# Performance work log

Measured on AMD Instinct MI355X. Metric: run time of the kernel, lower is better.

## Reference

```python
import jax, jax.numpy as jnp
import numpy as np

KERNEL_SIZE = 3
STRIDE = 1


def setup_inputs() -> dict:
    key = jax.random.key(0)
    k1, k2, k3 = jax.random.split(key, 3)
    B, Cin, Cout, L, K, S = 32, 128, 128, 2048, KERNEL_SIZE, STRIDE
    W = (L - 1) * S + K  # 2050
    x = jax.random.normal(k1, (B, Cin, W), dtype=jnp.float32)
    weight = jax.random.normal(k2, (Cout, Cin, L, K), dtype=jnp.float32) * 0.05
    bias = jax.random.normal(k3, (Cout, L), dtype=jnp.float32) * 0.05
    return {"x": x, "weight": weight, "bias": bias}


def reference(x, weight, bias):
    # x: (B, Cin, W); weight: (Cout, Cin, L, K); bias: (Cout, L)
    Cout, Cin, L, K = weight.shape
    # unfold: gather sliding windows -> (B, Cin, L, K)
    idx = jnp.arange(L)[:, None] * STRIDE + jnp.arange(K)[None, :]  # (L, K)
    patches = x[:, :, idx]  # (B, Cin, L, K)
    # per-position unshared contraction over (Cin, K)
    out = jnp.einsum('bclk,oclk->bol', patches, weight)  # (B, Cout, L)
    return out + bias[None, :, :]
```

## Files before the change

kernel.cpp:

```cpp
#include <hip/hip_runtime.h>


constexpr int CIN  = 128;
constexpr int COUT = 128;
constexpr int LL   = 2048;
constexpr int WID  = 2050;
constexpr int BATCH = 32;
constexpr int KK   = 3;

constexpr int O_TILE = 16;
constexpr int L_TILE = 16;
constexpr int CB = 4;
constexpr int TB = 4;
constexpr int TO = 2;
constexpr int TL = 4;
constexpr int J_USE = L_TILE + 2;
constexpr int J_PAD = 24;
constexpr int STAGE_PER_THREAD = (CB * BATCH * J_USE) / 256;

__global__ __launch_bounds__(256, 4)
void lc1d(const float* __restrict__ x, const float* __restrict__ w,
          const float* __restrict__ bias, float* __restrict__ out) {
  __shared__ float xs[CB * BATCH * J_PAD];

  const int tid = threadIdx.x;
  const int lg = tid & 3;
  const int og = (tid >> 2) & 7;
  const int bg = tid >> 5;

  const int bx = blockIdx.x;
  const int ltile = bx & 127;
  const int otile = bx >> 7;
  const int L0 = ltile * L_TILE;
  const int o_base = otile * O_TILE + og * TO;
  const int l_base = L0 + lg * TL;
  const int b_base = bg * TB;

  float acc[TB][TO][TL];
  #pragma unroll
  for (int oi = 0; oi < TO; ++oi) {
    const float4 bv =
        *reinterpret_cast<const float4*>(&bias[(o_base + oi) * LL + l_base]);
    #pragma unroll
    for (int bi = 0; bi < TB; ++bi) {
      acc[bi][oi][0] = bv.x; acc[bi][oi][1] = bv.y;
      acc[bi][oi][2] = bv.z; acc[bi][oi][3] = bv.w;
    }
  }

  int g_off[STAGE_PER_THREAD];
  int l_off[STAGE_PER_THREAD];
  #pragma unroll
  for (int i = 0; i < STAGE_PER_THREAD; ++i) {
    const int u  = tid + 256 * i;
    const int cs = u / (BATCH * J_USE);
    const int r  = u - cs * (BATCH * J_USE);
    const int b  = r / J_USE;
    const int j  = r - b * J_USE;
    g_off[i] = (b * CIN + cs) * WID + L0 + j;
    l_off[i] = (cs * BATCH + b) * J_PAD + j;
  }

  int w_off[TO];
  #pragma unroll
  for (int oi = 0; oi < TO; ++oi)
    w_off[oi] = (o_base + oi) * (CIN * LL * KK) + l_base * KK;

  for (int c0 = 0; c0 < CIN; c0 += CB) {
    __syncthreads();
    #pragma unroll
    for (int i = 0; i < STAGE_PER_THREAD; ++i) {
      xs[l_off[i]] = x[g_off[i]];
      g_off[i] += CB * WID;
    }
    __syncthreads();

    #pragma unroll
    for (int cs = 0; cs < CB; ++cs) {
      float4 wv[TO][3];
      #pragma unroll
      for (int oi = 0; oi < TO; ++oi) {
        const float* wp = w + (w_off[oi] + cs * (LL * KK));
        wv[oi][0] = *reinterpret_cast<const float4*>(wp);
        wv[oi][1] = *reinterpret_cast<const float4*>(wp + 4);
        wv[oi][2] = *reinterpret_cast<const float4*>(wp + 8);
      }
      #pragma unroll
      for (int bi = 0; bi < TB; ++bi) {
        const float* xr =
            &xs[(cs * BATCH + (b_base + bi)) * J_PAD + lg * TL];
        const float4 xa = *reinterpret_cast<const float4*>(xr);
        const float2 xb = *reinterpret_cast<const float2*>(xr + 4);
        const float xv[6] = {xa.x, xa.y, xa.z, xa.w, xb.x, xb.y};
        #pragma unroll
        for (int oi = 0; oi < TO; ++oi) {
          const float* wf = reinterpret_cast<const float*>(&wv[oi][0]);
          #pragma unroll
          for (int j = 0; j < TL; ++j) {
            #pragma unroll
            for (int k = 0; k < KK; ++k)
              acc[bi][oi][j] = fmaf(wf[j * KK + k], xv[j + k], acc[bi][oi][j]);
          }
        }
      }
    }
    #pragma unroll
    for (int oi = 0; oi < TO; ++oi) w_off[oi] += CB * (LL * KK);
  }

  #pragma unroll
  for (int bi = 0; bi < TB; ++bi) {
    const int b = b_base + bi;
    #pragma unroll
    for (int oi = 0; oi < TO; ++oi) {
      const float4 v = make_float4(acc[bi][oi][0], acc[bi][oi][1],
                                   acc[bi][oi][2], acc[bi][oi][3]);
      *reinterpret_cast<float4*>(&out[(b * COUT + (o_base + oi)) * LL + l_base]) = v;
    }
  }
}

extern "C" void kernel_launch(void* const* d_in, const int* in_sizes, int n_in,
                              void* d_out, int out_size, void* d_ws, size_t ws_size,
                              hipStream_t stream) {
  const float* x    = (const float*)d_in[0];
  const float* wgt  = (const float*)d_in[1];
  const float* bias = (const float*)d_in[2];
  float* out = (float*)d_out;
  hipLaunchKernelGGL(lc1d, dim3(1024), dim3(256), 0, stream, x, wgt, bias, out);
}
```

Before: 709.5 us.

## Replace LDS staging with register double-buffered direct loads and persistent grid

```diff
diff --git a/kernel.cpp b/kernel.cpp
--- a/kernel.cpp
+++ b/kernel.cpp
@@ -1,121 +1,125 @@
 #include <hip/hip_runtime.h>
 
 
-constexpr int CIN  = 128;
-constexpr int COUT = 128;
-constexpr int LL   = 2048;
-constexpr int WID  = 2050;
-constexpr int BATCH = 32;
-constexpr int KK   = 3;
+constexpr int CIN = 128;
+constexpr int LL  = 2048;
+constexpr int WID = 2050;
+constexpr int KK  = 3;
 
-constexpr int O_TILE = 16;
-constexpr int L_TILE = 16;
-constexpr int CB = 4;
 constexpr int TB = 4;
 constexpr int TO = 2;
 constexpr int TL = 4;
-constexpr int J_USE = L_TILE + 2;
-constexpr int J_PAD = 24;
-constexpr int STAGE_PER_THREAD = (CB * BATCH * J_USE) / 256;
+constexpr int WCS = LL * KK;
+constexpr int NTILE = 1024;
+constexpr int GRID = 768;
 
-__global__ __launch_bounds__(256, 4)
+struct WReg { float4 v[TO][3]; };
+struct XReg { float2 v[TB][3]; };
+
+__device__ __forceinline__ void load_w(const float* __restrict__ w,
+                                       const int* woff, int coff, WReg& r) {
+#pragma unroll
+  for (int oi = 0; oi < TO; ++oi) {
+    const float* p = w + woff[oi] + coff;
+    r.v[oi][0] = *reinterpret_cast<const float4*>(p);
+    r.v[oi][1] = *reinterpret_cast<const float4*>(p + 4);
+    r.v[oi][2] = *reinterpret_cast<const float4*>(p + 8);
+  }
+}
+
+__device__ __forceinline__ void load_x(const float* __restrict__ x,
+                                       const int* xoff, int coff, XReg& r) {
+#pragma unroll
+  for (int bi = 0; bi < TB; ++bi) {
+    const float* p = x + xoff[bi] + coff;
+    r.v[bi][0] = *reinterpret_cast<const float2*>(p);
+    r.v[bi][1] = *reinterpret_cast<const float2*>(p + 2);
+    r.v[bi][2] = *reinterpret_cast<const float2*>(p + 4);
+  }
+}
+
+__device__ __forceinline__ void compute(const WReg& wr, const XReg& xr,
+                                        float acc[TB][TO][TL]) {
+#pragma unroll
+  for (int bi = 0; bi < TB; ++bi) {
+    float xs[6];
+    xs[0] = xr.v[bi][0].x; xs[1] = xr.v[bi][0].y;
+    xs[2] = xr.v[bi][1].x; xs[3] = xr.v[bi][1].y;
+    xs[4] = xr.v[bi][2].x; xs[5] = xr.v[bi][2].y;
+#pragma unroll
+    for (int oi = 0; oi < TO; ++oi) {
+      const float* wf = reinterpret_cast<const float*>(&wr.v[oi][0]);
+#pragma unroll
+      for (int j = 0; j < TL; ++j)
+#pragma unroll
+        for (int k = 0; k < KK; ++k)
+          acc[bi][oi][j] = fmaf(wf[j * KK + k], xs[j + k], acc[bi][oi][j]);
+    }
+  }
+}
+
+__global__ __launch_bounds__(256, 3)
 void lc1d(const float* __restrict__ x, const float* __restrict__ w,
           const float* __restrict__ bias, float* __restrict__ out) {
-  __shared__ float xs[CB * BATCH * J_PAD];
-
   const int tid = threadIdx.x;
   const int lg = tid & 3;
   const int og = (tid >> 2) & 7;
   const int bg = tid >> 5;
 
-  const int bx = blockIdx.x;
-  const int ltile = bx & 127;
-  const int otile = bx >> 7;
-  const int L0 = ltile * L_TILE;
-  const int o_base = otile * O_TILE + og * TO;
-  const int l_base = L0 + lg * TL;
-  const int b_base = bg * TB;
+#pragma unroll 1
+  for (int tile = blockIdx.x; tile < NTILE; tile += GRID) {
+    const int L0 = (tile & 127) * 16;
+    const int o_base = (tile >> 7) * 16 + og * TO;
+    const int l_base = L0 + lg * TL;
+    const int b_base = bg * TB;
 
-  float acc[TB][TO][TL];
-  #pragma unroll
-  for (int oi = 0; oi < TO; ++oi) {
-    const float4 bv =
-        *reinterpret_cast<const float4*>(&bias[(o_base + oi) * LL + l_base]);
-    #pragma unroll
-    for (int bi = 0; bi < TB; ++bi) {
-      acc[bi][oi][0] = bv.x; acc[bi][oi][1] = bv.y;
-      acc[bi][oi][2] = bv.z; acc[bi][oi][3] = bv.w;
-    }
-  }
+    int woff[TO], xoff[TB];
+#pragma unroll
+    for (int oi = 0; oi < TO; ++oi)
+      woff[oi] = (o_base + oi) * (CIN * WCS) + l_base * KK;
+#pragma unroll
+    for (int bi = 0; bi < TB; ++bi)
+      xoff[bi] = (b_base + bi) * (CIN * WID) + l_base;
 
-  int g_off[STAGE_PER_THREAD];
-  int l_off[STAGE_PER_THREAD];
-  #pragma unroll
-  for (int i = 0; i < STAGE_PER_THREAD; ++i) {
-    const int u  = tid + 256 * i;
-    const int cs = u / (BATCH * J_USE);
-    const int r  = u - cs * (BATCH * J_USE);
-    const int b  = r / J_USE;
-    const int j  = r - b * J_USE;
-    g_off[i] = (b * CIN + cs) * WID + L0 + j;
-    l_off[i] = (cs * BATCH + b) * J_PAD + j;
-  }
-
-  int w_off[TO];
-  #pragma unroll
-  for (int oi = 0; oi < TO; ++oi)
-    w_off[oi] = (o_base + oi) * (CIN * LL * KK) + l_base * KK;
-
-  for (int c0 = 0; c0 < CIN; c0 += CB) {
-    __syncthreads();
-    #pragma unroll
-    for (int i = 0; i < STAGE_PER_THREAD; ++i) {
-      xs[l_off[i]] = x[g_off[i]];
-      g_off[i] += CB * WID;
-    }
-    __syncthreads();
-
-    #pragma unroll
-    for (int cs = 0; cs < CB; ++cs) {
-      float4 wv[TO][3];
-      #pragma unroll
-      for (int oi = 0; oi < TO; ++oi) {
-        const float* wp = w + (w_off[oi] + cs * (LL * KK));
-        wv[oi][0] = *reinterpret_cast<const float4*>(wp);
-        wv[oi][1] = *reinterpret_cast<const float4*>(wp + 4);
-        wv[oi][2] = *reinterpret_cast<const float4*>(wp + 8);
-      }
-      #pragma unroll
+    float acc[TB][TO][TL];
+#pragma unroll
+    for (int oi = 0; oi < TO; ++oi) {
+      const float4 bv =
+          *reinterpret_cast<const float4*>(&bias[(o_base + oi) * LL + l_base]);
+#pragma unroll
       for (int bi = 0; bi < TB; ++bi) {
-        const float* xr =
-            &xs[(cs * BATCH + (b_base + bi)) * J_PAD + lg * TL];
-        const float4 xa = *reinterpret_cast<const float4*>(xr);
-        const float2 xb = *reinterpret_cast<const float2*>(xr + 4);
-        const float xv[6] = {xa.x, xa.y, xa.z, xa.w, xb.x, xb.y};
-        #pragma unroll
-        for (int oi = 0; oi < TO; ++oi) {
-          const float* wf = reinterpret_cast<const float*>(&wv[oi][0]);
-          #pragma unroll
-          for (int j = 0; j < TL; ++j) {
-            #pragma unroll
-            for (int k = 0; k < KK; ++k)
-              acc[bi][oi][j] = fmaf(wf[j * KK + k], xv[j + k], acc[bi][oi][j]);
-          }
-        }
+        acc[bi][oi][0] = bv.x; acc[bi][oi][1] = bv.y;
+        acc[bi][oi][2] = bv.z; acc[bi][oi][3] = bv.w;
       }
     }
-    #pragma unroll
-    for (int oi = 0; oi < TO; ++oi) w_off[oi] += CB * (LL * KK);
-  }
 
-  #pragma unroll
-  for (int bi = 0; bi < TB; ++bi) {
-    const int b = b_base + bi;
-    #pragma unroll
-    for (int oi = 0; oi < TO; ++oi) {
-      const float4 v = make_float4(acc[bi][oi][0], acc[bi][oi][1],
-                                   acc[bi][oi][2], acc[bi][oi][3]);
-      *reinterpret_cast<float4*>(&out[(b * COUT + (o_base + oi)) * LL + l_base]) = v;
+    WReg wA, wB;
+    XReg xA, xB;
+    load_w(w, woff, 0, wA);        load_x(x, xoff, 0, xA);
+    load_w(w, woff, WCS, wB);      load_x(x, xoff, WID, xB);
+
+#pragma unroll 1
+    for (int c0 = 0; c0 < CIN; c0 += 2) {
+      const int cA = (c0 + 2 < CIN) ? (c0 + 2) : 0;
+      const int cB = (c0 + 3 < CIN) ? (c0 + 3) : 1;
+      compute(wA, xA, acc);
+      load_w(w, woff, cA * WCS, wA);
+      load_x(x, xoff, cA * WID, xA);
+      compute(wB, xB, acc);
+      load_w(w, woff, cB * WCS, wB);
+      load_x(x, xoff, cB * WID, xB);
+    }
+
+#pragma unroll
+    for (int bi = 0; bi < TB; ++bi) {
+      const int b = b_base + bi;
+#pragma unroll
+      for (int oi = 0; oi < TO; ++oi) {
+        const float4 v = make_float4(acc[bi][oi][0], acc[bi][oi][1],
+                                     acc[bi][oi][2], acc[bi][oi][3]);
+        *reinterpret_cast<float4*>(
+            &out[(b * CIN + (o_base + oi)) * LL + l_base]) = v;
+      }
     }
   }
 }
@@ -127,5 +131,5 @@
   const float* wgt  = (const float*)d_in[1];
   const float* bias = (const float*)d_in[2];
   float* out = (float*)d_out;
-  hipLaunchKernelGGL(lc1d, dim3(1024), dim3(256), 0, stream, x, wgt, bias, out);
+  hipLaunchKernelGGL(lc1d, dim3(GRID), dim3(256), 0, stream, x, wgt, bias, out);
 }
```

After: 887.0 us. 1.25x slower.
